# Kernel optimization log

Measured on AMD Instinct MI355X. Metric: run time of the kernel, lower is better.

The kernel has to match this reference:

```python
import jax, jax.numpy as jnp
import numpy as np

INITIAL_RADIUS = 1.0


def setup_inputs() -> dict:
    key = jax.random.key(0)
    k1, k2, k3 = jax.random.split(key, 3)
    B, N, S = 4, 8192, 2048
    xyz = jax.random.normal(k1, (B, 3, N), dtype=jnp.float32)
    sparse_xyz = jax.random.normal(k2, (B, 3, S), dtype=jnp.float32)
    sparse_flow = jax.random.normal(k3, (B, 3, S), dtype=jnp.float32)
    return {"xyz": xyz, "sparse_xyz": sparse_xyz, "sparse_flow": sparse_flow,
            "resol_factor": 1}


def reference(xyz, sparse_xyz, sparse_flow, resol_factor):
    # xyz: [B,3,N], sparse_xyz/sparse_flow: [B,3,S]
    radius = INITIAL_RADIUS * resol_factor
    x = jnp.transpose(xyz, (0, 2, 1))          # [B,N,3] dense query points
    y = jnp.transpose(sparse_xyz, (0, 2, 1))   # [B,S,3] sparse support points
    f = jnp.transpose(sparse_flow, (0, 2, 1))  # [B,S,3] sparse flow values
    B, S, _ = y.shape
    w = jnp.ones((B, S, 1), dtype=x.dtype)     # uniform sample weights

    # squared pairwise distances D2[b,n,s] = ||x_bn - y_bs||^2
    x2 = jnp.sum(x * x, axis=-1, keepdims=True)            # [B,N,1]
    y2 = jnp.sum(y * y, axis=-1)[:, None, :]               # [B,1,S]
    xy = jnp.einsum('bnd,bsd->bns', x, y)                  # [B,N,S]
    d2 = x2 + y2 - 2.0 * xy

    # Gaussian Nadaraya-Watson kernel weights
    k = jnp.exp(-d2 / (radius * radius))                   # [B,N,S]

    num = jnp.einsum('bns,bsd->bnd', k, f * w)             # [B,N,3]
    den = jnp.einsum('bns,bsd->bnd', k, w)                 # [B,N,1]
    dense = num / den                                      # [B,N,3]
    return jnp.transpose(dense, (0, 2, 1))                 # [B,3,N]
```

## Files before the change

### kernel.cpp

```cpp
#include <hip/hip_runtime.h>


typedef __attribute__((ext_vector_type(8))) float f8;

constexpr int B_ = 4, N_ = 8192, S_ = 2048;
constexpr int BLOCK = 256;
constexpr int NBPB = N_ / BLOCK;
constexpr int NB = B_ * NBPB;
constexpr int BN = B_ * N_;
constexpr float LOG2E = 1.4426950408889634f;

__global__ __launch_bounds__(BLOCK) void uf2_prep(
    const float* __restrict__ sxyz,
    const float* __restrict__ sflow,
    const int* __restrict__ resol,
    f8* __restrict__ P)
{
    const int i = blockIdx.x * BLOCK + threadIdx.x;
    const int b = i / S_;
    const int s = i - b * S_;
    const float r = (float)resol[0];
    const float inv_r2 = 1.0f / (r * r);
    const float c2 = 2.0f * inv_r2 * LOG2E;
    const float cy = -inv_r2 * LOG2E;
    const float* yb = sxyz  + b * 3 * S_;
    const float* fb = sflow + b * 3 * S_;
    const float yx = yb[s], yy = yb[S_ + s], yz = yb[2 * S_ + s];
    const float fx = fb[s], fy = fb[S_ + s], fz = fb[2 * S_ + s];
    const float ky = __builtin_amdgcn_exp2f(cy * (yx * yx + yy * yy + yz * yz));
    f8 v;
    v[0] = c2 * yx; v[1] = c2 * yy; v[2] = c2 * yz; v[3] = 0.0f;
    v[4] = ky * fx; v[5] = ky * fy; v[6] = ky * fz; v[7] = ky;
    P[i] = v;
}

template <int CHUNK>
__global__ __launch_bounds__(BLOCK) void uf2_main(
    const float* __restrict__ xyz,
    const f8* __restrict__ P,
    float4* __restrict__ part)
{
    const int nb = blockIdx.x % NB;
    const int sc = blockIdx.x / NB;
    const int b  = nb / NBPB;
    const int n  = (nb % NBPB) * BLOCK + threadIdx.x;

    const float* xb = xyz + b * 3 * N_;
    const float px = xb[n], py = xb[N_ + n], pz = xb[2 * N_ + n];

    const f8* __restrict__ p = P + b * S_ + sc * CHUNK;

    float ax = 0.f, ay = 0.f, az = 0.f, aw = 0.f;
#pragma unroll 8
    for (int t = 0; t < CHUNK; ++t) {
        const f8 v = p[t];
        float e = fmaf(px, v[0], fmaf(py, v[1], pz * v[2]));
        const float k = __builtin_amdgcn_exp2f(e);
        ax = fmaf(k, v[4], ax);
        ay = fmaf(k, v[5], ay);
        az = fmaf(k, v[6], az);
        aw = fmaf(k, v[7], aw);
    }

    const int g = b * N_ + n;
    part[(size_t)sc * BN + g] = make_float4(ax, ay, az, aw);
}

__global__ __launch_bounds__(BLOCK) void uf2_combine(
    const float4* __restrict__ part, float* __restrict__ out, int SC)
{
    const int g = blockIdx.x * BLOCK + threadIdx.x;
    float4 s = make_float4(0.f, 0.f, 0.f, 0.f);
    for (int c = 0; c < SC; ++c) {
        const float4 p = part[(size_t)c * BN + g];
        s.x += p.x; s.y += p.y; s.z += p.z; s.w += p.w;
    }
    const float inv = 1.0f / s.w;
    const int b = g >> 13;
    const int n = g & (N_ - 1);
    float* ob = out + b * 3 * N_;
    ob[n]          = s.x * inv;
    ob[N_ + n]     = s.y * inv;
    ob[2 * N_ + n] = s.z * inv;
}

__global__ __launch_bounds__(BLOCK, 1) void uf2_fused(
    const float* __restrict__ xyz,
    const float* __restrict__ sxyz,
    const float* __restrict__ sflow,
    const int* __restrict__ resol,
    float* __restrict__ out)
{
    constexpr int PPT = 4;
    constexpr int PTS = BLOCK * PPT;
    __shared__ float4 As[S_];
    __shared__ float4 Fs[S_];

    const int nb = blockIdx.x;
    const int b  = nb / (N_ / PTS);
    const int n0 = (nb % (N_ / PTS)) * PTS;

    const float r = (float)resol[0];
    const float inv_r2 = 1.0f / (r * r);
    const float c2 = 2.0f * inv_r2 * LOG2E;
    const float cy = -inv_r2 * LOG2E;

    const float* yb = sxyz  + b * 3 * S_;
    const float* fb = sflow + b * 3 * S_;
    for (int t = threadIdx.x; t < S_; t += BLOCK) {
        const float yx = yb[t], yy = yb[S_ + t], yz = yb[2 * S_ + t];
        const float fx = fb[t], fy = fb[S_ + t], fz = fb[2 * S_ + t];
        As[t] = make_float4(yx, yy, yz, cy * (yx * yx + yy * yy + yz * yz));
        Fs[t] = make_float4(fx, fy, fz, 0.0f);
    }
    __syncthreads();

    const float* xb = xyz + b * 3 * N_;
    float px[PPT], py[PPT], pz[PPT];
    float4 acc[PPT];
#pragma unroll
    for (int p = 0; p < PPT; ++p) {
        const int n = n0 + threadIdx.x + p * BLOCK;
        px[p] = xb[n]; py[p] = xb[N_ + n]; pz[p] = xb[2 * N_ + n];
        acc[p] = make_float4(0.f, 0.f, 0.f, 0.f);
    }
#pragma unroll 4
    for (int t = 0; t < S_; ++t) {
        const float4 a = As[t];
        const float4 f = Fs[t];
#pragma unroll
        for (int p = 0; p < PPT; ++p) {
            float dot = px[p] * a.x;
            dot = fmaf(py[p], a.y, dot);
            dot = fmaf(pz[p], a.z, dot);
            const float k = __builtin_amdgcn_exp2f(fmaf(dot, c2, a.w));
            acc[p].x = fmaf(k, f.x, acc[p].x);
            acc[p].y = fmaf(k, f.y, acc[p].y);
            acc[p].z = fmaf(k, f.z, acc[p].z);
            acc[p].w += k;
        }
    }
#pragma unroll
    for (int p = 0; p < PPT; ++p) {
        const int n = n0 + threadIdx.x + p * BLOCK;
        const float inv = 1.0f / acc[p].w;
        float* ob = out + b * 3 * N_;
        ob[n]          = acc[p].x * inv;
        ob[N_ + n]     = acc[p].y * inv;
        ob[2 * N_ + n] = acc[p].z * inv;
    }
}

extern "C" void kernel_launch(void* const* d_in, const int* in_sizes, int n_in,
                              void* d_out, int out_size, void* d_ws, size_t ws_size,
                              hipStream_t stream)
{
    const float* xyz   = (const float*)d_in[0];
    const float* sxyz  = (const float*)d_in[1];
    const float* sflow = (const float*)d_in[2];
    const int*   resol = (const int*)d_in[3];
    float* out = (float*)d_out;

    const size_t P_bytes = (size_t)1 << 20;
    const size_t per_chunk = (size_t)BN * sizeof(float4);
    int SC = 16;
    while (SC > 1 && P_bytes + (size_t)SC * per_chunk > ws_size) SC >>= 1;

    if (P_bytes + (size_t)SC * per_chunk > ws_size) {
        uf2_fused<<<dim3(BN / 1024), dim3(BLOCK), 0, stream>>>(
            xyz, sxyz, sflow, resol, out);
        return;
    }

    f8* P = (f8*)d_ws;
    float4* part = (float4*)((char*)d_ws + P_bytes);

    uf2_prep<<<dim3((B_ * S_) / BLOCK), dim3(BLOCK), 0, stream>>>(
        sxyz, sflow, resol, P);

    dim3 grid(NB * SC), blk(BLOCK);
    switch (SC) {
        case 16: uf2_main<S_ / 16><<<grid, blk, 0, stream>>>(xyz, P, part); break;
        case 8:  uf2_main<S_ / 8 ><<<grid, blk, 0, stream>>>(xyz, P, part); break;
        case 4:  uf2_main<S_ / 4 ><<<grid, blk, 0, stream>>>(xyz, P, part); break;
        case 2:  uf2_main<S_ / 2 ><<<grid, blk, 0, stream>>>(xyz, P, part); break;
        default: uf2_main<S_     ><<<grid, blk, 0, stream>>>(xyz, P, part); break;
    }
    uf2_combine<<<dim3(BN / BLOCK), dim3(BLOCK), 0, stream>>>(part, out, SC);
}
```

Measured before the change: 32.58 us.

## Fold prep into main kernel with LDS staging and packed 2-wide FMA over 8 points

Removes the separate prep kernel. Each main-kernel block now stages its chunk of support points and flow into shared memory and computes the squared-norm term inline. Each thread handles 8 query points, processed in pairs with 2-wide vector FMAs, so every LDS load is reused across more points and packed FP32 math can be used. The split count rises to 32. The trade-offs are higher register pressure, more partial results for the combine kernel to read, and the exp term is no longer pre-multiplied by the support weight (the flow is multiplied directly).

```diff
diff --git a/kernel.cpp b/kernel.cpp
--- a/kernel.cpp
+++ b/kernel.cpp
@@ -1,69 +1,95 @@
 #include <hip/hip_runtime.h>
 
 
-typedef __attribute__((ext_vector_type(8))) float f8;
+typedef float v2f __attribute__((ext_vector_type(2)));
 
 constexpr int B_ = 4, N_ = 8192, S_ = 2048;
-constexpr int BLOCK = 256;
-constexpr int NBPB = N_ / BLOCK;
+constexpr int BLOCK = 256, PPT = 8, NPAIR = PPT / 2;
+constexpr int PTS_PER_BLOCK = BLOCK * PPT;
+constexpr int NBPB = N_ / PTS_PER_BLOCK;
 constexpr int NB = B_ * NBPB;
 constexpr int BN = B_ * N_;
 constexpr float LOG2E = 1.4426950408889634f;
 
-__global__ __launch_bounds__(BLOCK) void uf2_prep(
+template <int CHUNK>
+__global__ __launch_bounds__(BLOCK, 2) void uf2_main(
+    const float* __restrict__ xyz,
     const float* __restrict__ sxyz,
     const float* __restrict__ sflow,
     const int* __restrict__ resol,
-    f8* __restrict__ P)
-{
-    const int i = blockIdx.x * BLOCK + threadIdx.x;
-    const int b = i / S_;
-    const int s = i - b * S_;
+    float4* __restrict__ part)
+{
+    __shared__ float4 As[CHUNK];
+    __shared__ float4 Fs[CHUNK];
+
+    const int nb = blockIdx.x % NB;
+    const int sc = blockIdx.x / NB;
+    const int b  = nb / NBPB;
+    const int n0 = (nb % NBPB) * PTS_PER_BLOCK;
+    const int s0 = sc * CHUNK;
+
     const float r = (float)resol[0];
     const float inv_r2 = 1.0f / (r * r);
     const float c2 = 2.0f * inv_r2 * LOG2E;
     const float cy = -inv_r2 * LOG2E;
+
     const float* yb = sxyz  + b * 3 * S_;
     const float* fb = sflow + b * 3 * S_;
-    const float yx = yb[s], yy = yb[S_ + s], yz = yb[2 * S_ + s];
-    const float fx = fb[s], fy = fb[S_ + s], fz = fb[2 * S_ + s];
-    const float ky = __builtin_amdgcn_exp2f(cy * (yx * yx + yy * yy + yz * yz));
-    f8 v;
-    v[0] = c2 * yx; v[1] = c2 * yy; v[2] = c2 * yz; v[3] = 0.0f;
-    v[4] = ky * fx; v[5] = ky * fy; v[6] = ky * fz; v[7] = ky;
-    P[i] = v;
-}
-
-template <int CHUNK>
-__global__ __launch_bounds__(BLOCK) void uf2_main(
-    const float* __restrict__ xyz,
-    const f8* __restrict__ P,
-    float4* __restrict__ part)
-{
-    const int nb = blockIdx.x % NB;
-    const int sc = blockIdx.x / NB;
-    const int b  = nb / NBPB;
-    const int n  = (nb % NBPB) * BLOCK + threadIdx.x;
+    for (int t = threadIdx.x; t < CHUNK; t += BLOCK) {
+        const int s = s0 + t;
+        const float yx = yb[s], yy = yb[S_ + s], yz = yb[2 * S_ + s];
+        const float fx = fb[s], fy = fb[S_ + s], fz = fb[2 * S_ + s];
+        As[t] = make_float4(c2 * yx, c2 * yy, c2 * yz,
+                            cy * (yx * yx + yy * yy + yz * yz));
+        Fs[t] = make_float4(fx, fy, fz, 0.0f);
+    }
+    __syncthreads();
 
     const float* xb = xyz + b * 3 * N_;
-    const float px = xb[n], py = xb[N_ + n], pz = xb[2 * N_ + n];
-
-    const f8* __restrict__ p = P + b * S_ + sc * CHUNK;
-
-    float ax = 0.f, ay = 0.f, az = 0.f, aw = 0.f;
-#pragma unroll 8
+    v2f px[NPAIR], py[NPAIR], pz[NPAIR];
+    v2f acx[NPAIR], acy[NPAIR], acz[NPAIR], acw[NPAIR];
+#pragma unroll
+    for (int q = 0; q < NPAIR; ++q) {
+        const int na = n0 + threadIdx.x + (2 * q) * BLOCK;
+        const int nbp = na + BLOCK;
+        px[q] = (v2f){xb[na], xb[nbp]};
+        py[q] = (v2f){xb[N_ + na], xb[N_ + nbp]};
+        pz[q] = (v2f){xb[2 * N_ + na], xb[2 * N_ + nbp]};
+        acx[q] = (v2f){0.f, 0.f}; acy[q] = (v2f){0.f, 0.f};
+        acz[q] = (v2f){0.f, 0.f}; acw[q] = (v2f){0.f, 0.f};
+    }
+
+#pragma unroll 2
     for (int t = 0; t < CHUNK; ++t) {
-        const f8 v = p[t];
-        float e = fmaf(px, v[0], fmaf(py, v[1], pz * v[2]));
-        const float k = __builtin_amdgcn_exp2f(e);
-        ax = fmaf(k, v[4], ax);
-        ay = fmaf(k, v[5], ay);
-        az = fmaf(k, v[6], az);
-        aw = fmaf(k, v[7], aw);
-    }
-
-    const int g = b * N_ + n;
-    part[(size_t)sc * BN + g] = make_float4(ax, ay, az, aw);
+        const float4 a = As[t];
+        const float4 f = Fs[t];
+        const v2f ax = (v2f){a.x, a.x}, ay = (v2f){a.y, a.y};
+        const v2f az = (v2f){a.z, a.z}, aw = (v2f){a.w, a.w};
+        const v2f fx = (v2f){f.x, f.x}, fy = (v2f){f.y, f.y};
+        const v2f fz = (v2f){f.z, f.z};
+#pragma unroll
+        for (int q = 0; q < NPAIR; ++q) {
+            v2f e = __builtin_elementwise_fma(pz[q], az, aw);
+            e = __builtin_elementwise_fma(py[q], ay, e);
+            e = __builtin_elementwise_fma(px[q], ax, e);
+            v2f k;
+            k.x = __builtin_amdgcn_exp2f(e.x);
+            k.y = __builtin_amdgcn_exp2f(e.y);
+            acx[q] = __builtin_elementwise_fma(k, fx, acx[q]);
+            acy[q] = __builtin_elementwise_fma(k, fy, acy[q]);
+            acz[q] = __builtin_elementwise_fma(k, fz, acz[q]);
+            acw[q] += k;
+        }
+    }
+
+#pragma unroll
+    for (int q = 0; q < NPAIR; ++q) {
+        const int ga = b * N_ + n0 + threadIdx.x + (2 * q) * BLOCK;
+        part[(size_t)sc * BN + ga] =
+            make_float4(acx[q].x, acy[q].x, acz[q].x, acw[q].x);
+        part[(size_t)sc * BN + ga + BLOCK] =
+            make_float4(acx[q].y, acy[q].y, acz[q].y, acw[q].y);
+    }
 }
 
 __global__ __launch_bounds__(BLOCK) void uf2_combine(
@@ -91,8 +117,8 @@
     const int* __restrict__ resol,
     float* __restrict__ out)
 {
-    constexpr int PPT = 4;
-    constexpr int PTS = BLOCK * PPT;
+    constexpr int FPPT = 4;
+    constexpr int PTS = BLOCK * FPPT;
     __shared__ float4 As[S_];
     __shared__ float4 Fs[S_];
 
@@ -110,16 +136,17 @@
     for (int t = threadIdx.x; t < S_; t += BLOCK) {
         const float yx = yb[t], yy = yb[S_ + t], yz = yb[2 * S_ + t];
         const float fx = fb[t], fy = fb[S_ + t], fz = fb[2 * S_ + t];
-        As[t] = make_float4(yx, yy, yz, cy * (yx * yx + yy * yy + yz * yz));
+        As[t] = make_float4(c2 * yx, c2 * yy, c2 * yz,
+                            cy * (yx * yx + yy * yy + yz * yz));
         Fs[t] = make_float4(fx, fy, fz, 0.0f);
     }
     __syncthreads();
 
     const float* xb = xyz + b * 3 * N_;
-    float px[PPT], py[PPT], pz[PPT];
-    float4 acc[PPT];
-#pragma unroll
-    for (int p = 0; p < PPT; ++p) {
+    float px[FPPT], py[FPPT], pz[FPPT];
+    float4 acc[FPPT];
+#pragma unroll
+    for (int p = 0; p < FPPT; ++p) {
         const int n = n0 + threadIdx.x + p * BLOCK;
         px[p] = xb[n]; py[p] = xb[N_ + n]; pz[p] = xb[2 * N_ + n];
         acc[p] = make_float4(0.f, 0.f, 0.f, 0.f);
@@ -129,11 +156,11 @@
         const float4 a = As[t];
         const float4 f = Fs[t];
 #pragma unroll
-        for (int p = 0; p < PPT; ++p) {
-            float dot = px[p] * a.x;
-            dot = fmaf(py[p], a.y, dot);
-            dot = fmaf(pz[p], a.z, dot);
-            const float k = __builtin_amdgcn_exp2f(fmaf(dot, c2, a.w));
+        for (int p = 0; p < FPPT; ++p) {
+            float e = fmaf(pz[p], a.z, a.w);
+            e = fmaf(py[p], a.y, e);
+            e = fmaf(px[p], a.x, e);
+            const float k = __builtin_amdgcn_exp2f(e);
             acc[p].x = fmaf(k, f.x, acc[p].x);
             acc[p].y = fmaf(k, f.y, acc[p].y);
             acc[p].z = fmaf(k, f.z, acc[p].z);
@@ -141,7 +168,7 @@
         }
     }
 #pragma unroll
-    for (int p = 0; p < PPT; ++p) {
+    for (int p = 0; p < FPPT; ++p) {
         const int n = n0 + threadIdx.x + p * BLOCK;
         const float inv = 1.0f / acc[p].w;
         float* ob = out + b * 3 * N_;
@@ -160,31 +187,26 @@
     const float* sflow = (const float*)d_in[2];
     const int*   resol = (const int*)d_in[3];
     float* out = (float*)d_out;
-
-    const size_t P_bytes = (size_t)1 << 20;
+    float4* part = (float4*)d_ws;
+
     const size_t per_chunk = (size_t)BN * sizeof(float4);
-    int SC = 16;
-    while (SC > 1 && P_bytes + (size_t)SC * per_chunk > ws_size) SC >>= 1;
-
-    if (P_bytes + (size_t)SC * per_chunk > ws_size) {
+    int SC = 32;
+    while (SC > 1 && (size_t)SC * per_chunk > ws_size) SC >>= 1;
+
+    if ((size_t)SC * per_chunk > ws_size) {
         uf2_fused<<<dim3(BN / 1024), dim3(BLOCK), 0, stream>>>(
             xyz, sxyz, sflow, resol, out);
         return;
     }
 
-    f8* P = (f8*)d_ws;
-    float4* part = (float4*)((char*)d_ws + P_bytes);
-
-    uf2_prep<<<dim3((B_ * S_) / BLOCK), dim3(BLOCK), 0, stream>>>(
-        sxyz, sflow, resol, P);
-
     dim3 grid(NB * SC), blk(BLOCK);
     switch (SC) {
-        case 16: uf2_main<S_ / 16><<<grid, blk, 0, stream>>>(xyz, P, part); break;
-        case 8:  uf2_main<S_ / 8 ><<<grid, blk, 0, stream>>>(xyz, P, part); break;
-        case 4:  uf2_main<S_ / 4 ><<<grid, blk, 0, stream>>>(xyz, P, part); break;
-        case 2:  uf2_main<S_ / 2 ><<<grid, blk, 0, stream>>>(xyz, P, part); break;
-        default: uf2_main<S_     ><<<grid, blk, 0, stream>>>(xyz, P, part); break;
+        case 32: uf2_main<S_ / 32><<<grid, blk, 0, stream>>>(xyz, sxyz, sflow, resol, part); break;
+        case 16: uf2_main<S_ / 16><<<grid, blk, 0, stream>>>(xyz, sxyz, sflow, resol, part); break;
+        case 8:  uf2_main<S_ / 8 ><<<grid, blk, 0, stream>>>(xyz, sxyz, sflow, resol, part); break;
+        case 4:  uf2_main<S_ / 4 ><<<grid, blk, 0, stream>>>(xyz, sxyz, sflow, resol, part); break;
+        case 2:  uf2_main<S_ / 2 ><<<grid, blk, 0, stream>>>(xyz, sxyz, sflow, resol, part); break;
+        default: uf2_main<S_     ><<<grid, blk, 0, stream>>>(xyz, sxyz, sflow, resol, part); break;
     }
     uf2_combine<<<dim3(BN / BLOCK), dim3(BLOCK), 0, stream>>>(part, out, SC);
 }
```

New measurement: 35.66 us. 9.4% more time.
